# Kernel tuning notes

Measured on AMD Instinct MI355X. Metric: run time of the kernel, lower is better.

The kernel has to match this reference:

```python
import jax, jax.numpy as jnp
import numpy as np

N_NODES = 100000
N_EDGES = 1200000
EMBED_DIM = 64
N_LAYERS = 3


def setup_inputs() -> dict:
    key = jax.random.key(0)
    k1, k2, k3, k4 = jax.random.split(key, 4)
    embeddings = jax.random.normal(k1, (N_NODES, EMBED_DIM), dtype=jnp.float32)
    edge_weight = jax.random.uniform(k2, (N_EDGES,), dtype=jnp.float32)
    edge_src = jax.random.randint(k3, (N_EDGES,), 0, N_NODES, dtype=jnp.int32)
    edge_dst = jax.random.randint(k4, (N_EDGES,), 0, N_NODES, dtype=jnp.int32)
    return {"embeddings": embeddings, "edge_weight": edge_weight,
            "edge_src": edge_src, "edge_dst": edge_dst}


def _spmm(edge_src, edge_dst, edge_weight, x):
    # (A @ x)[d] = sum_{e: dst(e)=d} w[e] * x[src(e)]  -- COO SpMM via gather + segment_sum
    msgs = edge_weight[:, None] * x[edge_src]  # [E, D]
    return jax.ops.segment_sum(msgs, edge_dst, num_segments=N_NODES)


def reference(embeddings, edge_weight, edge_src, edge_dst):
    all_embeddings = [embeddings]
    ego = embeddings
    for _ in range(N_LAYERS):
        ego = _spmm(edge_src, edge_dst, edge_weight, ego)
        all_embeddings.append(ego)
    # stack layer outputs: [n_layers+1, N, D]
    return jnp.stack(all_embeddings, axis=0)
```

## Files before the change

### kernel.cpp

```cpp
#include <hip/hip_runtime.h>


#define N_NODES 100000
#define DIM 64
#define SCAN_CHUNK 1024


__global__ void hist_kernel(const int* __restrict__ edst, int* __restrict__ deg, int E) {
    int e = blockIdx.x * blockDim.x + threadIdx.x;
    if (e < E) atomicAdd(&deg[edst[e]], 1);
}

__global__ void scan1_kernel(const int* __restrict__ deg, int* __restrict__ off,
                             int* __restrict__ bsum, int n) {
    __shared__ int sdata[256];
    int tid = threadIdx.x;
    int base = blockIdx.x * SCAN_CHUNK + tid * 4;
    int v[4];
    #pragma unroll
    for (int i = 0; i < 4; ++i) v[i] = (base + i < n) ? deg[base + i] : 0;
    int tsum = v[0] + v[1] + v[2] + v[3];
    sdata[tid] = tsum;
    __syncthreads();
    for (int d = 1; d < 256; d <<= 1) {
        int t = (tid >= d) ? sdata[tid - d] : 0;
        __syncthreads();
        sdata[tid] += t;
        __syncthreads();
    }
    int excl = sdata[tid] - tsum;
    if (tid == 255) bsum[blockIdx.x] = sdata[255];
    int run = excl;
    #pragma unroll
    for (int i = 0; i < 4; ++i) {
        if (base + i < n) off[base + i] = run;
        run += v[i];
    }
}

__global__ void scan2_kernel(int* __restrict__ bsum, int nb) {
    __shared__ int s[128];
    int tid = threadIdx.x;
    int v = (tid < nb) ? bsum[tid] : 0;
    s[tid] = v;
    __syncthreads();
    for (int d = 1; d < 128; d <<= 1) {
        int t = (tid >= d) ? s[tid - d] : 0;
        __syncthreads();
        s[tid] += t;
        __syncthreads();
    }
    if (tid < nb) bsum[tid] = s[tid] - v;
}

__global__ void scan3_kernel(int* __restrict__ off, const int* __restrict__ bsum, int n) {
    int i = blockIdx.x * blockDim.x + threadIdx.x;
    if (i < n) off[i] += bsum[i / SCAN_CHUNK];
}

__global__ void scatter_kernel(const int* __restrict__ esrc, const int* __restrict__ edst,
                               const float* __restrict__ ew, const int* __restrict__ off,
                               int* __restrict__ cur, int2* __restrict__ pairs, int E) {
    int e = blockIdx.x * blockDim.x + threadIdx.x;
    if (e >= E) return;
    int d = edst[e];
    int p = off[d] + atomicAdd(&cur[d], 1);
    int2 pr;
    pr.x = esrc[e];
    pr.y = __float_as_int(ew[e]);
    pairs[p] = pr;
}


__global__ void spmm_csr_kernel(const float* __restrict__ x,
                                const int2* __restrict__ pairs,
                                const int* __restrict__ off,
                                const int* __restrict__ deg,
                                float* __restrict__ y) {
    int gtid = blockIdx.x * blockDim.x + threadIdx.x;
    int node = gtid >> 6;
    int lane = threadIdx.x & 63;
    int q  = lane >> 4;
    int ql = lane & 15;
    if (node >= N_NODES) return;
    int s0 = off[node];
    int n  = deg[node];
    float4 acc = make_float4(0.f, 0.f, 0.f, 0.f);
    for (int k = q; k < n; k += 4) {
        int2 pr = pairs[s0 + k];
        float w = __int_as_float(pr.y);
        const float4* row = (const float4*)(x + (size_t)pr.x * DIM);
        float4 v = row[ql];
        acc.x += w * v.x;
        acc.y += w * v.y;
        acc.z += w * v.z;
        acc.w += w * v.w;
    }
    acc.x += __shfl_xor(acc.x, 16); acc.y += __shfl_xor(acc.y, 16);
    acc.z += __shfl_xor(acc.z, 16); acc.w += __shfl_xor(acc.w, 16);
    acc.x += __shfl_xor(acc.x, 32); acc.y += __shfl_xor(acc.y, 32);
    acc.z += __shfl_xor(acc.z, 32); acc.w += __shfl_xor(acc.w, 32);
    if (q == 0) {
        float4* yrow = (float4*)(y + (size_t)node * DIM);
        yrow[ql] = acc;
    }
}


__global__ void spmm_atomic_kernel(const float* __restrict__ x, const float* __restrict__ ew,
                                   const int* __restrict__ esrc, const int* __restrict__ edst,
                                   float* __restrict__ y, int n_edges) {
    long long tid = (long long)blockIdx.x * blockDim.x + threadIdx.x;
    int e = (int)(tid >> 6);
    int d = (int)(tid & 63);
    if (e >= n_edges) return;
    int s = esrc[e]; int t = edst[e]; float w = ew[e];
    atomicAdd(&y[(long long)t * DIM + d], w * x[(long long)s * DIM + d]);
}

extern "C" void kernel_launch(void* const* d_in, const int* in_sizes, int n_in,
                              void* d_out, int out_size, void* d_ws, size_t ws_size,
                              hipStream_t stream) {
    const float* emb  = (const float*)d_in[0];
    const float* ew   = (const float*)d_in[1];
    const int*   esrc = (const int*)d_in[2];
    const int*   edst = (const int*)d_in[3];
    float* out = (float*)d_out;

    const int E = in_sizes[1];
    const size_t layer_elems = (size_t)N_NODES * DIM;

    size_t need = (size_t)E * 8 + (size_t)3 * N_NODES * 4 + 512;
    hipMemcpyAsync(out, emb, layer_elems * sizeof(float), hipMemcpyDeviceToDevice, stream);

    if (ws_size >= need) {
        char* w = (char*)d_ws;
        int2* pairs = (int2*)w;
        int* deg  = (int*)(w + (size_t)E * 8);
        int* cur  = deg + N_NODES;
        int* off  = cur + N_NODES;
        int* bsum = off + N_NODES;

        hipMemsetAsync(deg, 0, (size_t)2 * N_NODES * 4, stream);

        const int eb = (E + 255) / 256;
        hist_kernel<<<eb, 256, 0, stream>>>(edst, deg, E);

        const int nscan = (N_NODES + SCAN_CHUNK - 1) / SCAN_CHUNK;
        scan1_kernel<<<nscan, 256, 0, stream>>>(deg, off, bsum, N_NODES);
        scan2_kernel<<<1, 128, 0, stream>>>(bsum, nscan);
        scan3_kernel<<<(N_NODES + 255) / 256, 256, 0, stream>>>(off, bsum, N_NODES);

        scatter_kernel<<<eb, 256, 0, stream>>>(esrc, edst, ew, off, cur, pairs, E);

        const int nb = (N_NODES + 3) / 4;
        for (int l = 1; l <= 3; ++l) {
            spmm_csr_kernel<<<nb, 256, 0, stream>>>(
                out + (size_t)(l - 1) * layer_elems, pairs, off, deg,
                out + (size_t)l * layer_elems);
        }
    } else {
        hipMemsetAsync(out + layer_elems, 0, 3 * layer_elems * sizeof(float), stream);
        const long long total_threads = (long long)E * 64;
        const int blocks = (int)((total_threads + 255) / 256);
        for (int l = 1; l <= 3; ++l) {
            spmm_atomic_kernel<<<blocks, 256, 0, stream>>>(
                out + (size_t)(l - 1) * layer_elems, ew, esrc, edst,
                out + (size_t)l * layer_elems, E);
        }
    }
}
```

Measured before the change: 398.6 us.

## Two-pass bucketed CSR build and octet-per-edge SpMM with two float4 loads

Replaces the single random scatter into CSR order with a two-pass binning. Edges are first bucketed by destination block of 128 nodes into a temp buffer placed in the unused output layers, then each bucket is scattered locally into final CSR positions. This aims to cut the cost of scattered global writes and atomics. The SpMM kernel now assigns 8 edges per wavefront iteration with each lane loading two float4s, which raises memory-level parallelism per wave but adds an extra shuffle reduction stage.

Result: slower. 919.4 us (+130.7%).

```diff
diff --git a/kernel.cpp b/kernel.cpp
--- a/kernel.cpp
+++ b/kernel.cpp
@@ -4,12 +4,41 @@
 #define N_NODES 100000
 #define DIM 64
 #define SCAN_CHUNK 1024
-
-
-__global__ void hist_kernel(const int* __restrict__ edst, int* __restrict__ deg, int E) {
+#define BSHIFT 7
+#define NB ((N_NODES + 127) / 128)
+
+
+__global__ void build_hist_kernel(const int* __restrict__ edst,
+                                  int* __restrict__ deg,
+                                  int* __restrict__ histB, int E) {
     int e = blockIdx.x * blockDim.x + threadIdx.x;
-    if (e < E) atomicAdd(&deg[edst[e]], 1);
-}
+    if (e >= E) return;
+    int d = edst[e];
+    atomicAdd(&deg[d], 1);
+    atomicAdd(&histB[d >> BSHIFT], 1);
+}
+
+
+__global__ void scanB_kernel(const int* __restrict__ histB,
+                             int* __restrict__ offB, int* __restrict__ curB) {
+    __shared__ int s[1024];
+    int tid = threadIdx.x;
+    int v = (tid < NB) ? histB[tid] : 0;
+    s[tid] = v;
+    __syncthreads();
+    for (int d = 1; d < 1024; d <<= 1) {
+        int t = (tid >= d) ? s[tid - d] : 0;
+        __syncthreads();
+        s[tid] += t;
+        __syncthreads();
+    }
+    if (tid < NB) {
+        int excl = s[tid] - v;
+        offB[tid] = excl;
+        curB[tid] = excl;
+    }
+}
+
 
 __global__ void scan1_kernel(const int* __restrict__ deg, int* __restrict__ off,
                              int* __restrict__ bsum, int n) {
@@ -58,51 +87,75 @@
     if (i < n) off[i] += bsum[i / SCAN_CHUNK];
 }
 
-__global__ void scatter_kernel(const int* __restrict__ esrc, const int* __restrict__ edst,
-                               const float* __restrict__ ew, const int* __restrict__ off,
-                               int* __restrict__ cur, int2* __restrict__ pairs, int E) {
+
+__global__ void binA_kernel(const int* __restrict__ esrc, const int* __restrict__ edst,
+                            const float* __restrict__ ew, int* __restrict__ curB,
+                            int2* __restrict__ tmp, int E) {
     int e = blockIdx.x * blockDim.x + threadIdx.x;
     if (e >= E) return;
     int d = edst[e];
-    int p = off[d] + atomicAdd(&cur[d], 1);
-    int2 pr;
-    pr.x = esrc[e];
-    pr.y = __float_as_int(ew[e]);
-    pairs[p] = pr;
-}
-
-
-__global__ void spmm_csr_kernel(const float* __restrict__ x,
-                                const int2* __restrict__ pairs,
-                                const int* __restrict__ off,
-                                const int* __restrict__ deg,
-                                float* __restrict__ y) {
+    int b = d >> BSHIFT;
+    int p = atomicAdd(&curB[b], 1);
+    int2 t;
+    t.x = (esrc[e] << BSHIFT) | (d & 127);
+    t.y = __float_as_int(ew[e]);
+    tmp[p] = t;
+}
+
+
+__global__ void binB_kernel(const int2* __restrict__ tmp,
+                            const int* __restrict__ offB, const int* __restrict__ histB,
+                            const int* __restrict__ off, int* __restrict__ cur,
+                            int2* __restrict__ pairs) {
+    int b = blockIdx.x;
+    int start = offB[b];
+    int cnt = histB[b];
+    for (int i = threadIdx.x; i < cnt; i += blockDim.x) {
+        int2 t = tmp[start + i];
+        int dst = (b << BSHIFT) | (t.x & 127);
+        int src = t.x >> BSHIFT;
+        int p = off[dst] + atomicAdd(&cur[dst], 1);
+        int2 pr; pr.x = src; pr.y = t.y;
+        pairs[p] = pr;
+    }
+}
+
+
+__global__ void spmm_octet_kernel(const float* __restrict__ x,
+                                  const int2* __restrict__ pairs,
+                                  const int* __restrict__ off,
+                                  const int* __restrict__ deg,
+                                  float* __restrict__ y) {
     int gtid = blockIdx.x * blockDim.x + threadIdx.x;
     int node = gtid >> 6;
     int lane = threadIdx.x & 63;
-    int q  = lane >> 4;
-    int ql = lane & 15;
+    int oct = lane >> 3;
+    int ol  = lane & 7;
     if (node >= N_NODES) return;
     int s0 = off[node];
     int n  = deg[node];
-    float4 acc = make_float4(0.f, 0.f, 0.f, 0.f);
-    for (int k = q; k < n; k += 4) {
+    float4 a0 = make_float4(0.f, 0.f, 0.f, 0.f);
+    float4 a1 = make_float4(0.f, 0.f, 0.f, 0.f);
+    for (int k = oct; k < n; k += 8) {
         int2 pr = pairs[s0 + k];
         float w = __int_as_float(pr.y);
         const float4* row = (const float4*)(x + (size_t)pr.x * DIM);
-        float4 v = row[ql];
-        acc.x += w * v.x;
-        acc.y += w * v.y;
-        acc.z += w * v.z;
-        acc.w += w * v.w;
-    }
-    acc.x += __shfl_xor(acc.x, 16); acc.y += __shfl_xor(acc.y, 16);
-    acc.z += __shfl_xor(acc.z, 16); acc.w += __shfl_xor(acc.w, 16);
-    acc.x += __shfl_xor(acc.x, 32); acc.y += __shfl_xor(acc.y, 32);
-    acc.z += __shfl_xor(acc.z, 32); acc.w += __shfl_xor(acc.w, 32);
-    if (q == 0) {
+        float4 v0 = row[2 * ol];
+        float4 v1 = row[2 * ol + 1];
+        a0.x += w * v0.x; a0.y += w * v0.y; a0.z += w * v0.z; a0.w += w * v0.w;
+        a1.x += w * v1.x; a1.y += w * v1.y; a1.z += w * v1.z; a1.w += w * v1.w;
+    }
+    #pragma unroll
+    for (int d = 8; d < 64; d <<= 1) {
+        a0.x += __shfl_xor(a0.x, d); a0.y += __shfl_xor(a0.y, d);
+        a0.z += __shfl_xor(a0.z, d); a0.w += __shfl_xor(a0.w, d);
+        a1.x += __shfl_xor(a1.x, d); a1.y += __shfl_xor(a1.y, d);
+        a1.z += __shfl_xor(a1.z, d); a1.w += __shfl_xor(a1.w, d);
+    }
+    if (oct == 0) {
         float4* yrow = (float4*)(y + (size_t)node * DIM);
-        yrow[ql] = acc;
+        yrow[2 * ol]     = a0;
+        yrow[2 * ol + 1] = a1;
     }
 }
 
@@ -130,32 +183,41 @@
     const int E = in_sizes[1];
     const size_t layer_elems = (size_t)N_NODES * DIM;
 
-    size_t need = (size_t)E * 8 + (size_t)3 * N_NODES * 4 + 512;
+    size_t need = (size_t)E * 8 +
+                  ((size_t)3 * N_NODES + NB * 3 + 128 + 16) * 4;
+
     hipMemcpyAsync(out, emb, layer_elems * sizeof(float), hipMemcpyDeviceToDevice, stream);
 
     if (ws_size >= need) {
         char* w = (char*)d_ws;
         int2* pairs = (int2*)w;
-        int* deg  = (int*)(w + (size_t)E * 8);
-        int* cur  = deg + N_NODES;
-        int* off  = cur + N_NODES;
-        int* bsum = off + N_NODES;
-
-        hipMemsetAsync(deg, 0, (size_t)2 * N_NODES * 4, stream);
+        int* deg   = (int*)(w + (size_t)E * 8);
+        int* cur   = deg + N_NODES;
+        int* histB = cur + N_NODES;
+        int* off   = histB + NB;
+        int* bsum  = off + N_NODES;
+        int* offB  = bsum + 128;
+        int* curB  = offB + NB;
+        int2* tmp = (int2*)(out + layer_elems);
+
+        hipMemsetAsync(deg, 0, ((size_t)2 * N_NODES + NB) * 4, stream);
 
         const int eb = (E + 255) / 256;
-        hist_kernel<<<eb, 256, 0, stream>>>(edst, deg, E);
+        build_hist_kernel<<<eb, 256, 0, stream>>>(edst, deg, histB, E);
+
+        scanB_kernel<<<1, 1024, 0, stream>>>(histB, offB, curB);
 
         const int nscan = (N_NODES + SCAN_CHUNK - 1) / SCAN_CHUNK;
         scan1_kernel<<<nscan, 256, 0, stream>>>(deg, off, bsum, N_NODES);
         scan2_kernel<<<1, 128, 0, stream>>>(bsum, nscan);
         scan3_kernel<<<(N_NODES + 255) / 256, 256, 0, stream>>>(off, bsum, N_NODES);
 
-        scatter_kernel<<<eb, 256, 0, stream>>>(esrc, edst, ew, off, cur, pairs, E);
+        binA_kernel<<<eb, 256, 0, stream>>>(esrc, edst, ew, curB, tmp, E);
+        binB_kernel<<<NB, 256, 0, stream>>>(tmp, offB, histB, off, cur, pairs);
 
         const int nb = (N_NODES + 3) / 4;
         for (int l = 1; l <= 3; ++l) {
-            spmm_csr_kernel<<<nb, 256, 0, stream>>>(
+            spmm_octet_kernel<<<nb, 256, 0, stream>>>(
                 out + (size_t)(l - 1) * layer_elems, pairs, off, deg,
                 out + (size_t)l * layer_elems);
         }
```
